# Performance work log

Measured on AMD Instinct MI355X. Metric: run time of the kernel, lower is better.

The kernel has to match this reference:

```python
import jax, jax.numpy as jnp
import numpy as np

N_HEAD = 12

def fillnan(x):
    return jnp.nan_to_num(x, nan=0.0, posinf=0.0, neginf=0.0)

def setup_inputs() -> dict:
    key = jax.random.key(0)
    k1, k2, k3 = jax.random.split(key, 3)
    B, T, C = 2, 2048, 768
    x = jax.random.normal(k1, (B, T, C), dtype=jnp.float32)
    W_attn = jax.random.normal(k2, (3 * C, C), dtype=jnp.float32) * 0.02
    W_proj = jax.random.normal(k3, (C, C), dtype=jnp.float32) * 0.02
    return {"x": x, "W_attn": W_attn, "W_proj": W_proj}

def reference(x, W_attn, W_proj):
    B, T, C = x.shape
    H = N_HEAD
    D = C // H
    # qkv projection (torch Linear: x @ W^T), then nan-sanitize
    qkv = fillnan(jnp.einsum('btc,fc->btf', x, W_attn))  # [B,T,3C]
    q, k, v = jnp.split(qkv, 3, axis=-1)
    # [B,T,C] -> [B,H,T,D]
    q = q.reshape(B, T, H, D).transpose(0, 2, 1, 3)
    k = k.reshape(B, T, H, D).transpose(0, 2, 1, 3)
    v = v.reshape(B, T, H, D).transpose(0, 2, 1, 3)
    scale = 1.0 / np.sqrt(D).astype(np.float32)
    att = jnp.einsum('bhqd,bhkd->bhqk', q, k) * scale  # [B,H,T,T]
    att = fillnan(att)
    causal = jnp.tril(jnp.ones((T, T), dtype=bool))
    att = jnp.where(causal[None, None], att, -jnp.inf)
    att = jax.nn.softmax(att, axis=-1)
    att = fillnan(att)
    y = jnp.einsum('bhqk,bhkd->bhqd', att, v)  # [B,H,T,D]
    y = fillnan(y)
    y = y.transpose(0, 2, 1, 3).reshape(B, T, C)
    y = fillnan(jnp.einsum('btc,fc->btf', y, W_proj))
    return y
```

## Files before the change

kernel.cpp:

```cpp
#include <hip/hip_runtime.h>

typedef __attribute__((ext_vector_type(8))) short bf16x8;
typedef __attribute__((ext_vector_type(4))) float f32x4;

__device__ __forceinline__ unsigned short f2b(float f) {
  union { float f; unsigned u; } v; v.f = f;
  return (unsigned short)((v.u + 0x7FFFu + ((v.u >> 16) & 1u)) >> 16);
}
__device__ __forceinline__ unsigned short f2b_fast(float f) {
  union { float f; unsigned u; } v; v.f = f;
  return (unsigned short)((v.u + 0x8000u) >> 16);
}

#define XN4   786432
#define WAN4  442368
#define WPN4  147456
__global__ void cvt_all(const float* __restrict__ x, const float* __restrict__ Wa,
                        const float* __restrict__ Wp,
                        unsigned short* __restrict__ xb, unsigned short* __restrict__ Wab,
                        unsigned short* __restrict__ Wpb) {
  int i = blockIdx.x * 256 + threadIdx.x;
  const float* src; unsigned short* dst; int off;
  if (i < XN4)            { src = x;  dst = xb;  off = i; }
  else if (i < XN4 + WAN4){ src = Wa; dst = Wab; off = i - XN4; }
  else                    { src = Wp; dst = Wpb; off = i - XN4 - WAN4; }
  float4 f = reinterpret_cast<const float4*>(src)[off];
  ushort4 o;
  o.x = f2b(f.x); o.y = f2b(f.y); o.z = f2b(f.z); o.w = f2b(f.w);
  reinterpret_cast<ushort4*>(dst)[off] = o;
}

#define BK 64

__global__ __launch_bounds__(256, 2)
void gemm_qkv(const unsigned short* __restrict__ A,
              const unsigned short* __restrict__ Bm,
              unsigned short* __restrict__ qb,
              unsigned short* __restrict__ kb_,
              unsigned short* __restrict__ vt) {
  __shared__ unsigned short As[128 * 64];
  __shared__ unsigned short Bs[128 * 64];
  const int K = 768;
  int tid = threadIdx.x;
  int wave = tid >> 6, lane = tid & 63;
  int quad = lane >> 4, l16 = lane & 15;
  int m0 = blockIdx.x * 128, n0 = blockIdx.y * 128;
  int wm = (wave & 1) * 64, wn = (wave >> 1) * 64;
  bool vswap = (n0 >= 1536);

  int srow = lane >> 3;
  int scol = ((lane & 7) ^ srow) << 3;

  f32x4 acc[4][4] = {};

  for (int k0 = 0; k0 < K; k0 += BK) {
    __syncthreads();
#pragma unroll
    for (int i = 0; i < 4; ++i) {
      int r = wave * 32 + i * 8;
      __builtin_amdgcn_global_load_lds(
          (const __attribute__((address_space(1))) unsigned int*)(A + (size_t)(m0 + r + srow) * K + k0 + scol),
          (__attribute__((address_space(3))) unsigned int*)(As + r * 64), 16, 0, 0);
      __builtin_amdgcn_global_load_lds(
          (const __attribute__((address_space(1))) unsigned int*)(Bm + (size_t)(n0 + r + srow) * K + k0 + scol),
          (__attribute__((address_space(3))) unsigned int*)(Bs + r * 64), 16, 0, 0);
    }
    __syncthreads();
#pragma unroll
    for (int kb = 0; kb < 2; ++kb) {
      int ch = (((kb << 2) | quad) ^ (l16 & 7)) << 3;
      bf16x8 af[4], bf[4];
#pragma unroll
      for (int i = 0; i < 4; ++i)
        af[i] = *reinterpret_cast<const bf16x8*>(As + (wm + i * 16 + l16) * 64 + ch);
#pragma unroll
      for (int j = 0; j < 4; ++j)
        bf[j] = *reinterpret_cast<const bf16x8*>(Bs + (wn + j * 16 + l16) * 64 + ch);
      if (!vswap) {
#pragma unroll
        for (int i = 0; i < 4; ++i)
#pragma unroll
          for (int j = 0; j < 4; ++j)
            acc[i][j] = __builtin_amdgcn_mfma_f32_16x16x32_bf16(af[i], bf[j], acc[i][j], 0, 0, 0);
      } else {
#pragma unroll
        for (int i = 0; i < 4; ++i)
#pragma unroll
          for (int j = 0; j < 4; ++j)
            acc[i][j] = __builtin_amdgcn_mfma_f32_16x16x32_bf16(bf[j], af[i], acc[i][j], 0, 0, 0);
      }
    }
  }

  const float scale2 = 0.125f * 1.44269504089f;
  if (!vswap) {
#pragma unroll
    for (int i = 0; i < 4; ++i) {
      int mbase = m0 + wm + i * 16 + quad * 4;
#pragma unroll
      for (int j = 0; j < 4; ++j) {
        int f = n0 + wn + j * 16 + l16;
        int which = f / 768;
        int f2 = f - which * 768;
        int h = f2 >> 6, d = f2 & 63;
#pragma unroll
        for (int r = 0; r < 4; ++r) {
          int m = mbase + r;
          int b = m >> 11, t = m & 2047;
          int bh = b * 12 + h;
          if (which == 0) qb[((size_t)(bh * 2048 + t)) * 64 + d] = f2b(acc[i][j][r] * scale2);
          else            kb_[((size_t)(bh * 2048 + t)) * 64 + d] = f2b(acc[i][j][r]);
        }
      }
    }
  } else {
#pragma unroll
    for (int j = 0; j < 4; ++j) {
      int fbase = n0 + wn + j * 16 + quad * 4 - 1536;
#pragma unroll
      for (int i = 0; i < 4; ++i) {
        int t_g = m0 + wm + i * 16 + l16;
        int b = t_g >> 11, t = t_g & 2047;
#pragma unroll
        for (int r = 0; r < 4; ++r) {
          int f2 = fbase + r;
          int h = f2 >> 6, d = f2 & 63;
          int bh = b * 12 + h;
          vt[((size_t)(bh * 64 + d)) * 2048 + t] = f2b(acc[i][j][r]);
        }
      }
    }
  }
}

#define CK 512

__global__ __launch_bounds__(256, 4)
void attn_part(const unsigned short* __restrict__ Qb,
               const unsigned short* __restrict__ Kb,
               const unsigned short* __restrict__ Vt,
               float* __restrict__ Oacc, float* __restrict__ Lacc) {
  __shared__ unsigned short Ks[64 * 64];
  __shared__ unsigned short Vs[64 * 64];
  __shared__ unsigned short P[4 * 32 * 64];
  const int T = 2048, D = 64;
  int wave = threadIdx.x >> 6, lane = threadIdx.x & 63;
  int quad = lane >> 4, l16 = lane & 15;

  int w = blockIdx.x;
  int bh = w / 40;
  int r = w - bh * 40;
  int b = 15;
#pragma unroll
  for (int i = 0; i < 16; ++i) {
    int nb = (i >> 2) + 1;
    if (r < nb) { b = i; break; }
    r -= nb;
  }
  int c = r;
  int q0 = b * 128;
  int qrow = q0 + wave * 32;
  int kbeg = c * CK;
  int kend = kbeg + CK; if (kend > q0 + 128) kend = q0 + 128;

  const unsigned short* Qp = Qb + (size_t)bh * T * D;
  const unsigned short* Kp = Kb + (size_t)bh * T * D;
  const unsigned short* Vp = Vt + (size_t)bh * D * T;
  unsigned short* Pw = P + wave * 32 * 64;

  int srow = lane >> 3;
  int scol = ((lane & 7) ^ srow) << 3;

  bf16x8 aq[2][2];
#pragma unroll
  for (int qi = 0; qi < 2; ++qi)
#pragma unroll
    for (int cc = 0; cc < 2; ++cc)
      aq[qi][cc] = *reinterpret_cast<const bf16x8*>(
          Qp + (qrow + qi * 16 + l16) * D + cc * 32 + quad * 8);

  bf16x8 ones;
#pragma unroll
  for (int e = 0; e < 8; ++e) ones[e] = (short)0x3F80;

  f32x4 o[2][4] = {};
  f32x4 lacc[2] = {};
  int pswr = (l16 & 7) ^ (l16 >> 3);

  for (int k0 = kbeg; k0 < kend; k0 += 64) {
    __syncthreads();
#pragma unroll
    for (int i = 0; i < 2; ++i) {
      int rr = wave * 16 + i * 8;
      __builtin_amdgcn_global_load_lds(
          (const __attribute__((address_space(1))) unsigned int*)(Kp + (size_t)(k0 + rr + srow) * D + scol),
          (__attribute__((address_space(3))) unsigned int*)(Ks + rr * 64), 16, 0, 0);
      __builtin_amdgcn_global_load_lds(
          (const __attribute__((address_space(1))) unsigned int*)(Vp + (size_t)(rr + srow) * T + k0 + scol),
          (__attribute__((address_space(3))) unsigned int*)(Vs + rr * 64), 16, 0, 0);
    }
    __syncthreads();

    if (k0 > qrow + 31) continue;

    f32x4 sacc[2][4] = {};
#pragma unroll
    for (int nt = 0; nt < 4; ++nt) {
      bf16x8 bk0 = *reinterpret_cast<const bf16x8*>(Ks + (nt * 16 + l16) * 64 + ((quad ^ (l16 & 7)) << 3));
      bf16x8 bk1 = *reinterpret_cast<const bf16x8*>(Ks + (nt * 16 + l16) * 64 + (((4 | quad) ^ (l16 & 7)) << 3));
#pragma unroll
      for (int qi = 0; qi < 2; ++qi) {
        sacc[qi][nt] = __builtin_amdgcn_mfma_f32_16x16x32_bf16(aq[qi][0], bk0, sacc[qi][nt], 0, 0, 0);
        sacc[qi][nt] = __builtin_amdgcn_mfma_f32_16x16x32_bf16(aq[qi][1], bk1, sacc[qi][nt], 0, 0, 0);
      }
    }

    if (k0 + 63 > qrow) {
#pragma unroll
      for (int qi = 0; qi < 2; ++qi)
#pragma unroll
        for (int nt = 0; nt < 4; ++nt) {
          int col = k0 + nt * 16 + l16;
#pragma unroll
          for (int rr = 0; rr < 4; ++rr) {
            int row = qrow + qi * 16 + quad * 4 + rr;
            sacc[qi][nt][rr] = (col <= row) ? sacc[qi][nt][rr] : -1e30f;
          }
        }
    }
#pragma unroll
    for (int qi = 0; qi < 2; ++qi)
#pragma unroll
      for (int nt = 0; nt < 4; ++nt)
#pragma unroll
        for (int rr = 0; rr < 4; ++rr)
          sacc[qi][nt][rr] = exp2f(sacc[qi][nt][rr]);

#pragma unroll
    for (int qi = 0; qi < 2; ++qi)
#pragma unroll
      for (int rr = 0; rr < 4; ++rr) {
        int prow = qi * 16 + quad * 4 + rr;
        int psw = (prow & 7) ^ ((prow >> 3) & 1);
#pragma unroll
        for (int nt = 0; nt < 4; ++nt)
          Pw[prow * 64 + (((nt * 2 + (l16 >> 3)) ^ psw) << 3) + (l16 & 7)] = f2b_fast(sacc[qi][nt][rr]);
      }
    __asm__ volatile("s_waitcnt lgkmcnt(0)" ::: "memory");

    bf16x8 vf[4][2];
#pragma unroll
    for (int dt = 0; dt < 4; ++dt) {
      vf[dt][0] = *reinterpret_cast<const bf16x8*>(Vs + (dt * 16 + l16) * 64 + ((quad ^ (l16 & 7)) << 3));
      vf[dt][1] = *reinterpret_cast<const bf16x8*>(Vs + (dt * 16 + l16) * 64 + (((4 | quad) ^ (l16 & 7)) << 3));
    }
#pragma unroll
    for (int qi = 0; qi < 2; ++qi) {
      bf16x8 ap0 = *reinterpret_cast<const bf16x8*>(Pw + (qi * 16 + l16) * 64 + ((quad ^ pswr) << 3));
      bf16x8 ap1 = *reinterpret_cast<const bf16x8*>(Pw + (qi * 16 + l16) * 64 + (((4 | quad) ^ pswr) << 3));
#pragma unroll
      for (int dt = 0; dt < 4; ++dt) {
        o[qi][dt] = __builtin_amdgcn_mfma_f32_16x16x32_bf16(ap0, vf[dt][0], o[qi][dt], 0, 0, 0);
        o[qi][dt] = __builtin_amdgcn_mfma_f32_16x16x32_bf16(ap1, vf[dt][1], o[qi][dt], 0, 0, 0);
      }
      lacc[qi] = __builtin_amdgcn_mfma_f32_16x16x32_bf16(ap0, ones, lacc[qi], 0, 0, 0);
      lacc[qi] = __builtin_amdgcn_mfma_f32_16x16x32_bf16(ap1, ones, lacc[qi], 0, 0, 0);
    }
  }

#pragma unroll
  for (int qi = 0; qi < 2; ++qi)
#pragma unroll
    for (int dt = 0; dt < 4; ++dt)
#pragma unroll
      for (int rr = 0; rr < 4; ++rr) {
        int row = qrow + qi * 16 + quad * 4 + rr;
        atomicAdd(&Oacc[((size_t)(bh * T + row)) * 64 + dt * 16 + l16], o[qi][dt][rr]);
      }
  if (l16 == 0) {
#pragma unroll
    for (int qi = 0; qi < 2; ++qi)
#pragma unroll
      for (int rr = 0; rr < 4; ++rr)
        atomicAdd(&Lacc[bh * T + qrow + qi * 16 + quad * 4 + rr], lacc[qi][rr]);
  }
}

__global__ __launch_bounds__(256, 2)
void gemm_proj(const float* __restrict__ Oacc, const float* __restrict__ Lacc,
               const unsigned short* __restrict__ Wpb, float* __restrict__ out) {
  __shared__ unsigned short As[64 * 64];
  __shared__ unsigned short Bs[128 * 64];
  int tid = threadIdx.x;
  int wave = tid >> 6, lane = tid & 63;
  int quad = lane >> 4, l16 = lane & 15;
  int m0 = blockIdx.x * 64, n0 = blockIdx.y * 128;
  int wm = (wave & 1) * 32, wn = (wave >> 1) * 64;

  int srow = lane >> 3;
  int scol = ((lane & 7) ^ srow) << 3;

  int arow = tid >> 2;
  int acg = (tid & 3) * 2;
  int t_g = m0 + arow;
  int bb = t_g >> 11, tt = t_g & 2047;
  int asw = arow & 7;

  f32x4 acc[2][4] = {};

  for (int k0 = 0; k0 < 768; k0 += BK) {
    int h = k0 >> 6;
    const float* arp = Oacc + ((size_t)((bb * 12 + h) * 2048 + tt)) * 64 + acg * 8;
    float rl = 1.0f / Lacc[(bb * 12 + h) * 2048 + tt];
    float4 a0 = reinterpret_cast<const float4*>(arp)[0];
    float4 a1 = reinterpret_cast<const float4*>(arp)[1];
    float4 a2 = reinterpret_cast<const float4*>(arp)[2];
    float4 a3 = reinterpret_cast<const float4*>(arp)[3];

    __syncthreads();
#pragma unroll
    for (int i = 0; i < 4; ++i) {
      int r = wave * 32 + i * 8;
      __builtin_amdgcn_global_load_lds(
          (const __attribute__((address_space(1))) unsigned int*)(Wpb + (size_t)(n0 + r + srow) * 768 + k0 + scol),
          (__attribute__((address_space(3))) unsigned int*)(Bs + r * 64), 16, 0, 0);
    }
    bf16x8 p0, p1;
    p0[0] = (short)f2b(a0.x * rl); p0[1] = (short)f2b(a0.y * rl);
    p0[2] = (short)f2b(a0.z * rl); p0[3] = (short)f2b(a0.w * rl);
    p0[4] = (short)f2b(a1.x * rl); p0[5] = (short)f2b(a1.y * rl);
    p0[6] = (short)f2b(a1.z * rl); p0[7] = (short)f2b(a1.w * rl);
    p1[0] = (short)f2b(a2.x * rl); p1[1] = (short)f2b(a2.y * rl);
    p1[2] = (short)f2b(a2.z * rl); p1[3] = (short)f2b(a2.w * rl);
    p1[4] = (short)f2b(a3.x * rl); p1[5] = (short)f2b(a3.y * rl);
    p1[6] = (short)f2b(a3.z * rl); p1[7] = (short)f2b(a3.w * rl);
    *reinterpret_cast<bf16x8*>(As + arow * 64 + ((acg ^ asw) << 3)) = p0;
    *reinterpret_cast<bf16x8*>(As + arow * 64 + (((acg + 1) ^ asw) << 3)) = p1;
    __syncthreads();

#pragma unroll
    for (int kb = 0; kb < 2; ++kb) {
      int ch = (((kb << 2) | quad) ^ (l16 & 7)) << 3;
      bf16x8 af[2], bf[4];
#pragma unroll
      for (int i = 0; i < 2; ++i)
        af[i] = *reinterpret_cast<const bf16x8*>(As + (wm + i * 16 + l16) * 64 + ch);
#pragma unroll
      for (int j = 0; j < 4; ++j)
        bf[j] = *reinterpret_cast<const bf16x8*>(Bs + (wn + j * 16 + l16) * 64 + ch);
#pragma unroll
      for (int i = 0; i < 2; ++i)
#pragma unroll
        for (int j = 0; j < 4; ++j)
          acc[i][j] = __builtin_amdgcn_mfma_f32_16x16x32_bf16(af[i], bf[j], acc[i][j], 0, 0, 0);
    }
  }

#pragma unroll
  for (int i = 0; i < 2; ++i) {
    int mbase = m0 + wm + i * 16 + quad * 4;
#pragma unroll
    for (int j = 0; j < 4; ++j) {
      int col = n0 + wn + j * 16 + l16;
#pragma unroll
      for (int r = 0; r < 4; ++r)
        out[(size_t)(mbase + r) * 768 + col] = acc[i][j][r];
    }
  }
}

extern "C" void kernel_launch(void* const* d_in, const int* in_sizes, int n_in,
                              void* d_out, int out_size, void* d_ws, size_t ws_size,
                              hipStream_t stream) {
  const float* x  = (const float*)d_in[0];
  const float* Wa = (const float*)d_in[1];
  const float* Wp = (const float*)d_in[2];
  float* out = (float*)d_out;

  unsigned short* ws = (unsigned short*)d_ws;
  unsigned short* xb  = ws;
  unsigned short* Wab = xb  + 3145728;
  unsigned short* Wpb = Wab + 1769472;
  unsigned short* Qb  = Wpb + 589824;
  unsigned short* Kb  = Qb  + 3145728;
  unsigned short* Vt  = Kb  + 3145728;
  float*          Oacc = (float*)(Vt + 3145728);
  float*          Lacc = Oacc + 3145728;

  hipMemsetAsync(Oacc, 0, (3145728 + 49152) * sizeof(float), stream);

  cvt_all<<<(XN4 + WAN4 + WPN4) / 256, 256, 0, stream>>>(x, Wa, Wp, xb, Wab, Wpb);

  gemm_qkv<<<dim3(32, 18), 256, 0, stream>>>(xb, Wab, Qb, Kb, Vt);

  attn_part<<<960, 256, 0, stream>>>(Qb, Kb, Vt, Oacc, Lacc);

  gemm_proj<<<dim3(64, 6), 256, 0, stream>>>(Oacc, Lacc, Wpb, out);
}
```

Before: 185.2 us.

## Double-buffer LDS in all GEMM and attention kernels; finer attention split with XCD mapping

Adds double-buffered shared-memory staging to the QKV GEMM, attention and projection GEMM kernels. Each kernel now prefetches the next K tile while computing on the current one, which removes one barrier per iteration. The attention key-chunk size is halved (CK 256), giving 1728 blocks, and blockIdx is remapped so heads are grouped per XCD for L2 locality. The risks are higher LDS use, which lowers occupancy (launch bounds reduced to 3), and more partial-sum atomics into Oacc from the finer split.

```diff
diff --git a/kernel.cpp b/kernel.cpp
--- a/kernel.cpp
+++ b/kernel.cpp
@@ -30,16 +30,14 @@
   reinterpret_cast<ushort4*>(dst)[off] = o;
 }
 
-#define BK 64
-
 __global__ __launch_bounds__(256, 2)
 void gemm_qkv(const unsigned short* __restrict__ A,
               const unsigned short* __restrict__ Bm,
               unsigned short* __restrict__ qb,
               unsigned short* __restrict__ kb_,
               unsigned short* __restrict__ vt) {
-  __shared__ unsigned short As[128 * 64];
-  __shared__ unsigned short Bs[128 * 64];
+  __shared__ unsigned short As[2][128 * 64];
+  __shared__ unsigned short Bs[2][128 * 64];
   const int K = 768;
   int tid = threadIdx.x;
   int wave = tid >> 6, lane = tid & 63;
@@ -51,31 +49,36 @@
   int srow = lane >> 3;
   int scol = ((lane & 7) ^ srow) << 3;
 
-  f32x4 acc[4][4] = {};
-
-  for (int k0 = 0; k0 < K; k0 += BK) {
-    __syncthreads();
+  auto stage = [&](int k0, int buf) {
 #pragma unroll
     for (int i = 0; i < 4; ++i) {
       int r = wave * 32 + i * 8;
       __builtin_amdgcn_global_load_lds(
           (const __attribute__((address_space(1))) unsigned int*)(A + (size_t)(m0 + r + srow) * K + k0 + scol),
-          (__attribute__((address_space(3))) unsigned int*)(As + r * 64), 16, 0, 0);
+          (__attribute__((address_space(3))) unsigned int*)(&As[buf][r * 64]), 16, 0, 0);
       __builtin_amdgcn_global_load_lds(
           (const __attribute__((address_space(1))) unsigned int*)(Bm + (size_t)(n0 + r + srow) * K + k0 + scol),
-          (__attribute__((address_space(3))) unsigned int*)(Bs + r * 64), 16, 0, 0);
-    }
+          (__attribute__((address_space(3))) unsigned int*)(&Bs[buf][r * 64]), 16, 0, 0);
+    }
+  };
+
+  f32x4 acc[4][4] = {};
+  stage(0, 0);
+  int cur = 0;
+
+  for (int k0 = 0; k0 < K; k0 += 64) {
     __syncthreads();
+    if (k0 + 64 < K) stage(k0 + 64, cur ^ 1);
 #pragma unroll
     for (int kb = 0; kb < 2; ++kb) {
       int ch = (((kb << 2) | quad) ^ (l16 & 7)) << 3;
       bf16x8 af[4], bf[4];
 #pragma unroll
       for (int i = 0; i < 4; ++i)
-        af[i] = *reinterpret_cast<const bf16x8*>(As + (wm + i * 16 + l16) * 64 + ch);
+        af[i] = *reinterpret_cast<const bf16x8*>(&As[cur][(wm + i * 16 + l16) * 64 + ch]);
 #pragma unroll
       for (int j = 0; j < 4; ++j)
-        bf[j] = *reinterpret_cast<const bf16x8*>(Bs + (wn + j * 16 + l16) * 64 + ch);
+        bf[j] = *reinterpret_cast<const bf16x8*>(&Bs[cur][(wn + j * 16 + l16) * 64 + ch]);
       if (!vswap) {
 #pragma unroll
         for (int i = 0; i < 4; ++i)
@@ -90,6 +93,7 @@
             acc[i][j] = __builtin_amdgcn_mfma_f32_16x16x32_bf16(bf[j], af[i], acc[i][j], 0, 0, 0);
       }
     }
+    cur ^= 1;
   }
 
   const float scale2 = 0.125f * 1.44269504089f;
@@ -133,27 +137,29 @@
   }
 }
 
-#define CK 512
-
-__global__ __launch_bounds__(256, 4)
+#define CK 256
+
+__global__ __launch_bounds__(256, 3)
 void attn_part(const unsigned short* __restrict__ Qb,
                const unsigned short* __restrict__ Kb,
                const unsigned short* __restrict__ Vt,
                float* __restrict__ Oacc, float* __restrict__ Lacc) {
-  __shared__ unsigned short Ks[64 * 64];
-  __shared__ unsigned short Vs[64 * 64];
+  __shared__ unsigned short Ks[2][64 * 64];
+  __shared__ unsigned short Vs[2][64 * 64];
   __shared__ unsigned short P[4 * 32 * 64];
   const int T = 2048, D = 64;
   int wave = threadIdx.x >> 6, lane = threadIdx.x & 63;
   int quad = lane >> 4, l16 = lane & 15;
 
-  int w = blockIdx.x;
-  int bh = w / 40;
-  int r = w - bh * 40;
+  int flat = blockIdx.x;
+  int xcd = flat & 7;
+  int ix = flat >> 3;
+  int bh = xcd * 3 + ix / 72;
+  int r = ix % 72;
   int b = 15;
 #pragma unroll
   for (int i = 0; i < 16; ++i) {
-    int nb = (i >> 2) + 1;
+    int nb = (i >> 1) + 1;
     if (r < nb) { b = i; break; }
     r -= nb;
   }
@@ -171,101 +177,109 @@
   int srow = lane >> 3;
   int scol = ((lane & 7) ^ srow) << 3;
 
-  bf16x8 aq[2][2];
-#pragma unroll
-  for (int qi = 0; qi < 2; ++qi)
-#pragma unroll
-    for (int cc = 0; cc < 2; ++cc)
-      aq[qi][cc] = *reinterpret_cast<const bf16x8*>(
-          Qp + (qrow + qi * 16 + l16) * D + cc * 32 + quad * 8);
-
-  bf16x8 ones;
-#pragma unroll
-  for (int e = 0; e < 8; ++e) ones[e] = (short)0x3F80;
-
-  f32x4 o[2][4] = {};
-  f32x4 lacc[2] = {};
-  int pswr = (l16 & 7) ^ (l16 >> 3);
-
-  for (int k0 = kbeg; k0 < kend; k0 += 64) {
-    __syncthreads();
+  auto stage = [&](int k0, int buf) {
 #pragma unroll
     for (int i = 0; i < 2; ++i) {
       int rr = wave * 16 + i * 8;
       __builtin_amdgcn_global_load_lds(
           (const __attribute__((address_space(1))) unsigned int*)(Kp + (size_t)(k0 + rr + srow) * D + scol),
-          (__attribute__((address_space(3))) unsigned int*)(Ks + rr * 64), 16, 0, 0);
+          (__attribute__((address_space(3))) unsigned int*)(&Ks[buf][rr * 64]), 16, 0, 0);
       __builtin_amdgcn_global_load_lds(
           (const __attribute__((address_space(1))) unsigned int*)(Vp + (size_t)(rr + srow) * T + k0 + scol),
-          (__attribute__((address_space(3))) unsigned int*)(Vs + rr * 64), 16, 0, 0);
-    }
+          (__attribute__((address_space(3))) unsigned int*)(&Vs[buf][rr * 64]), 16, 0, 0);
+    }
+  };
+
+  bf16x8 aq[2][2];
+#pragma unroll
+  for (int qi = 0; qi < 2; ++qi)
+#pragma unroll
+    for (int cc = 0; cc < 2; ++cc)
+      aq[qi][cc] = *reinterpret_cast<const bf16x8*>(
+          Qp + (qrow + qi * 16 + l16) * D + cc * 32 + quad * 8);
+
+  bf16x8 ones;
+#pragma unroll
+  for (int e = 0; e < 8; ++e) ones[e] = (short)0x3F80;
+
+  f32x4 o[2][4] = {};
+  f32x4 lacc[2] = {};
+  int pswr = (l16 & 7) ^ (l16 >> 3);
+
+  stage(kbeg, 0);
+  int cur = 0;
+
+  for (int k0 = kbeg; k0 < kend; k0 += 64) {
     __syncthreads();
-
-    if (k0 > qrow + 31) continue;
-
-    f32x4 sacc[2][4] = {};
-#pragma unroll
-    for (int nt = 0; nt < 4; ++nt) {
-      bf16x8 bk0 = *reinterpret_cast<const bf16x8*>(Ks + (nt * 16 + l16) * 64 + ((quad ^ (l16 & 7)) << 3));
-      bf16x8 bk1 = *reinterpret_cast<const bf16x8*>(Ks + (nt * 16 + l16) * 64 + (((4 | quad) ^ (l16 & 7)) << 3));
+    if (k0 + 64 < kend) stage(k0 + 64, cur ^ 1);
+
+    if (k0 <= qrow + 31) {
+      f32x4 sacc[2][4] = {};
+#pragma unroll
+      for (int nt = 0; nt < 4; ++nt) {
+        bf16x8 bk0 = *reinterpret_cast<const bf16x8*>(&Ks[cur][(nt * 16 + l16) * 64 + ((quad ^ (l16 & 7)) << 3)]);
+        bf16x8 bk1 = *reinterpret_cast<const bf16x8*>(&Ks[cur][(nt * 16 + l16) * 64 + (((4 | quad) ^ (l16 & 7)) << 3)]);
+#pragma unroll
+        for (int qi = 0; qi < 2; ++qi) {
+          sacc[qi][nt] = __builtin_amdgcn_mfma_f32_16x16x32_bf16(aq[qi][0], bk0, sacc[qi][nt], 0, 0, 0);
+          sacc[qi][nt] = __builtin_amdgcn_mfma_f32_16x16x32_bf16(aq[qi][1], bk1, sacc[qi][nt], 0, 0, 0);
+        }
+      }
+
+      if (k0 + 63 > qrow) {
+#pragma unroll
+        for (int qi = 0; qi < 2; ++qi)
+#pragma unroll
+          for (int nt = 0; nt < 4; ++nt) {
+            int col = k0 + nt * 16 + l16;
+#pragma unroll
+            for (int rr = 0; rr < 4; ++rr) {
+              int row = qrow + qi * 16 + quad * 4 + rr;
+              sacc[qi][nt][rr] = (col <= row) ? sacc[qi][nt][rr] : -1e30f;
+            }
+          }
+      }
+#pragma unroll
+      for (int qi = 0; qi < 2; ++qi)
+#pragma unroll
+        for (int nt = 0; nt < 4; ++nt)
+#pragma unroll
+          for (int rr = 0; rr < 4; ++rr)
+            sacc[qi][nt][rr] = exp2f(sacc[qi][nt][rr]);
+
+#pragma unroll
+      for (int qi = 0; qi < 2; ++qi)
+#pragma unroll
+        for (int rr = 0; rr < 4; ++rr) {
+          int prow = qi * 16 + quad * 4 + rr;
+          int psw = (prow & 7) ^ ((prow >> 3) & 1);
+#pragma unroll
+          for (int nt = 0; nt < 4; ++nt)
+            Pw[prow * 64 + (((nt * 2 + (l16 >> 3)) ^ psw) << 3) + (l16 & 7)] = f2b_fast(sacc[qi][nt][rr]);
+        }
+      __asm__ volatile("s_waitcnt lgkmcnt(0)" ::: "memory");
+
+      bf16x8 vf[4][2];
+#pragma unroll
+      for (int dt = 0; dt < 4; ++dt) {
+        vf[dt][0] = *reinterpret_cast<const bf16x8*>(&Vs[cur][(dt * 16 + l16) * 64 + ((quad ^ (l16 & 7)) << 3)]);
+        vf[dt][1] = *reinterpret_cast<const bf16x8*>(&Vs[cur][(dt * 16 + l16) * 64 + (((4 | quad) ^ (l16 & 7)) << 3)]);
+      }
 #pragma unroll
       for (int qi = 0; qi < 2; ++qi) {
-        sacc[qi][nt] = __builtin_amdgcn_mfma_f32_16x16x32_bf16(aq[qi][0], bk0, sacc[qi][nt], 0, 0, 0);
-        sacc[qi][nt] = __builtin_amdgcn_mfma_f32_16x16x32_bf16(aq[qi][1], bk1, sacc[qi][nt], 0, 0, 0);
-      }
-    }
-
-    if (k0 + 63 > qrow) {
-#pragma unroll
-      for (int qi = 0; qi < 2; ++qi)
-#pragma unroll
-        for (int nt = 0; nt < 4; ++nt) {
-          int col = k0 + nt * 16 + l16;
-#pragma unroll
-          for (int rr = 0; rr < 4; ++rr) {
-            int row = qrow + qi * 16 + quad * 4 + rr;
-            sacc[qi][nt][rr] = (col <= row) ? sacc[qi][nt][rr] : -1e30f;
-          }
+        bf16x8 ap0 = *reinterpret_cast<const bf16x8*>(Pw + (qi * 16 + l16) * 64 + ((quad ^ pswr) << 3));
+        bf16x8 ap1 = *reinterpret_cast<const bf16x8*>(Pw + (qi * 16 + l16) * 64 + (((4 | quad) ^ pswr) << 3));
+#pragma unroll
+        for (int dt = 0; dt < 4; ++dt) {
+          o[qi][dt] = __builtin_amdgcn_mfma_f32_16x16x32_bf16(ap0, vf[dt][0], o[qi][dt], 0, 0, 0);
+          o[qi][dt] = __builtin_amdgcn_mfma_f32_16x16x32_bf16(ap1, vf[dt][1], o[qi][dt], 0, 0, 0);
         }
-    }
-#pragma unroll
-    for (int qi = 0; qi < 2; ++qi)
-#pragma unroll
-      for (int nt = 0; nt < 4; ++nt)
-#pragma unroll
-        for (int rr = 0; rr < 4; ++rr)
-          sacc[qi][nt][rr] = exp2f(sacc[qi][nt][rr]);
-
-#pragma unroll
-    for (int qi = 0; qi < 2; ++qi)
-#pragma unroll
-      for (int rr = 0; rr < 4; ++rr) {
-        int prow = qi * 16 + quad * 4 + rr;
-        int psw = (prow & 7) ^ ((prow >> 3) & 1);
-#pragma unroll
-        for (int nt = 0; nt < 4; ++nt)
-          Pw[prow * 64 + (((nt * 2 + (l16 >> 3)) ^ psw) << 3) + (l16 & 7)] = f2b_fast(sacc[qi][nt][rr]);
-      }
-    __asm__ volatile("s_waitcnt lgkmcnt(0)" ::: "memory");
-
-    bf16x8 vf[4][2];
-#pragma unroll
-    for (int dt = 0; dt < 4; ++dt) {
-      vf[dt][0] = *reinterpret_cast<const bf16x8*>(Vs + (dt * 16 + l16) * 64 + ((quad ^ (l16 & 7)) << 3));
-      vf[dt][1] = *reinterpret_cast<const bf16x8*>(Vs + (dt * 16 + l16) * 64 + (((4 | quad) ^ (l16 & 7)) << 3));
-    }
-#pragma unroll
-    for (int qi = 0; qi < 2; ++qi) {
-      bf16x8 ap0 = *reinterpret_cast<const bf16x8*>(Pw + (qi * 16 + l16) * 64 + ((quad ^ pswr) << 3));
-      bf16x8 ap1 = *reinterpret_cast<const bf16x8*>(Pw + (qi * 16 + l16) * 64 + (((4 | quad) ^ pswr) << 3));
-#pragma unroll
-      for (int dt = 0; dt < 4; ++dt) {
-        o[qi][dt] = __builtin_amdgcn_mfma_f32_16x16x32_bf16(ap0, vf[dt][0], o[qi][dt], 0, 0, 0);
-        o[qi][dt] = __builtin_amdgcn_mfma_f32_16x16x32_bf16(ap1, vf[dt][1], o[qi][dt], 0, 0, 0);
-      }
-      lacc[qi] = __builtin_amdgcn_mfma_f32_16x16x32_bf16(ap0, ones, lacc[qi], 0, 0, 0);
-      lacc[qi] = __builtin_amdgcn_mfma_f32_16x16x32_bf16(ap1, ones, lacc[qi], 0, 0, 0);
-    }
+        lacc[qi] = __builtin_amdgcn_mfma_f32_16x16x32_bf16(ap0, ones, lacc[qi], 0, 0, 0);
+        lacc[qi] = __builtin_amdgcn_mfma_f32_16x16x32_bf16(ap1, ones, lacc[qi], 0, 0, 0);
+      }
+      __asm__ volatile("" ::: "memory");
+    }
+    cur ^= 1;
   }
 
 #pragma unroll
@@ -289,8 +303,8 @@
 __global__ __launch_bounds__(256, 2)
 void gemm_proj(const float* __restrict__ Oacc, const float* __restrict__ Lacc,
                const unsigned short* __restrict__ Wpb, float* __restrict__ out) {
-  __shared__ unsigned short As[64 * 64];
-  __shared__ unsigned short Bs[128 * 64];
+  __shared__ unsigned short As[2][64 * 64];
+  __shared__ unsigned short Bs[2][128 * 64];
   int tid = threadIdx.x;
   int wave = tid >> 6, lane = tid & 63;
   int quad = lane >> 4, l16 = lane & 15;
@@ -306,54 +320,72 @@
   int bb = t_g >> 11, tt = t_g & 2047;
   int asw = arow & 7;
 
-  f32x4 acc[2][4] = {};
-
-  for (int k0 = 0; k0 < 768; k0 += BK) {
-    int h = k0 >> 6;
-    const float* arp = Oacc + ((size_t)((bb * 12 + h) * 2048 + tt)) * 64 + acg * 8;
-    float rl = 1.0f / Lacc[(bb * 12 + h) * 2048 + tt];
-    float4 a0 = reinterpret_cast<const float4*>(arp)[0];
-    float4 a1 = reinterpret_cast<const float4*>(arp)[1];
-    float4 a2 = reinterpret_cast<const float4*>(arp)[2];
-    float4 a3 = reinterpret_cast<const float4*>(arp)[3];
-
-    __syncthreads();
+  auto stageB = [&](int k0, int buf) {
 #pragma unroll
     for (int i = 0; i < 4; ++i) {
       int r = wave * 32 + i * 8;
       __builtin_amdgcn_global_load_lds(
           (const __attribute__((address_space(1))) unsigned int*)(Wpb + (size_t)(n0 + r + srow) * 768 + k0 + scol),
-          (__attribute__((address_space(3))) unsigned int*)(Bs + r * 64), 16, 0, 0);
-    }
+          (__attribute__((address_space(3))) unsigned int*)(&Bs[buf][r * 64]), 16, 0, 0);
+    }
+  };
+  auto loadA = [&](int k0, float4* a, float& rl) {
+    int h = k0 >> 6;
+    const float* arp = Oacc + ((size_t)((bb * 12 + h) * 2048 + tt)) * 64 + acg * 8;
+    rl = 1.0f / Lacc[(bb * 12 + h) * 2048 + tt];
+    a[0] = reinterpret_cast<const float4*>(arp)[0];
+    a[1] = reinterpret_cast<const float4*>(arp)[1];
+    a[2] = reinterpret_cast<const float4*>(arp)[2];
+    a[3] = reinterpret_cast<const float4*>(arp)[3];
+  };
+  auto writeA = [&](const float4* a, float rl, int buf) {
     bf16x8 p0, p1;
-    p0[0] = (short)f2b(a0.x * rl); p0[1] = (short)f2b(a0.y * rl);
-    p0[2] = (short)f2b(a0.z * rl); p0[3] = (short)f2b(a0.w * rl);
-    p0[4] = (short)f2b(a1.x * rl); p0[5] = (short)f2b(a1.y * rl);
-    p0[6] = (short)f2b(a1.z * rl); p0[7] = (short)f2b(a1.w * rl);
-    p1[0] = (short)f2b(a2.x * rl); p1[1] = (short)f2b(a2.y * rl);
-    p1[2] = (short)f2b(a2.z * rl); p1[3] = (short)f2b(a2.w * rl);
-    p1[4] = (short)f2b(a3.x * rl); p1[5] = (short)f2b(a3.y * rl);
-    p1[6] = (short)f2b(a3.z * rl); p1[7] = (short)f2b(a3.w * rl);
-    *reinterpret_cast<bf16x8*>(As + arow * 64 + ((acg ^ asw) << 3)) = p0;
-    *reinterpret_cast<bf16x8*>(As + arow * 64 + (((acg + 1) ^ asw) << 3)) = p1;
+    p0[0] = (short)f2b(a[0].x * rl); p0[1] = (short)f2b(a[0].y * rl);
+    p0[2] = (short)f2b(a[0].z * rl); p0[3] = (short)f2b(a[0].w * rl);
+    p0[4] = (short)f2b(a[1].x * rl); p0[5] = (short)f2b(a[1].y * rl);
+    p0[6] = (short)f2b(a[1].z * rl); p0[7] = (short)f2b(a[1].w * rl);
+    p1[0] = (short)f2b(a[2].x * rl); p1[1] = (short)f2b(a[2].y * rl);
+    p1[2] = (short)f2b(a[2].z * rl); p1[3] = (short)f2b(a[2].w * rl);
+    p1[4] = (short)f2b(a[3].x * rl); p1[5] = (short)f2b(a[3].y * rl);
+    p1[6] = (short)f2b(a[3].z * rl); p1[7] = (short)f2b(a[3].w * rl);
+    *reinterpret_cast<bf16x8*>(&As[buf][arow * 64 + ((acg ^ asw) << 3)]) = p0;
+    *reinterpret_cast<bf16x8*>(&As[buf][arow * 64 + (((acg + 1) ^ asw) << 3)]) = p1;
+  };
+
+  f32x4 acc[2][4] = {};
+
+  float4 aP[4], aN[4];
+  float rlP, rlN;
+  stageB(0, 0);
+  loadA(0, aP, rlP);
+  loadA(64, aN, rlN);
+  writeA(aP, rlP, 0);
+  int cur = 0;
+
+  for (int k0 = 0; k0 < 768; k0 += 64) {
     __syncthreads();
-
+    if (k0 + 64 < 768) {
+      stageB(k0 + 64, cur ^ 1);
+      writeA(aN, rlN, cur ^ 1);
+      if (k0 + 128 < 768) loadA(k0 + 128, aN, rlN);
+    }
 #pragma unroll
     for (int kb = 0; kb < 2; ++kb) {
       int ch = (((kb << 2) | quad) ^ (l16 & 7)) << 3;
       bf16x8 af[2], bf[4];
 #pragma unroll
       for (int i = 0; i < 2; ++i)
-        af[i] = *reinterpret_cast<const bf16x8*>(As + (wm + i * 16 + l16) * 64 + ch);
+        af[i] = *reinterpret_cast<const bf16x8*>(&As[cur][(wm + i * 16 + l16) * 64 + ch]);
 #pragma unroll
       for (int j = 0; j < 4; ++j)
-        bf[j] = *reinterpret_cast<const bf16x8*>(Bs + (wn + j * 16 + l16) * 64 + ch);
+        bf[j] = *reinterpret_cast<const bf16x8*>(&Bs[cur][(wn + j * 16 + l16) * 64 + ch]);
 #pragma unroll
       for (int i = 0; i < 2; ++i)
 #pragma unroll
         for (int j = 0; j < 4; ++j)
           acc[i][j] = __builtin_amdgcn_mfma_f32_16x16x32_bf16(af[i], bf[j], acc[i][j], 0, 0, 0);
     }
+    cur ^= 1;
   }
 
 #pragma unroll
@@ -393,7 +425,7 @@
 
   gemm_qkv<<<dim3(32, 18), 256, 0, stream>>>(xb, Wab, Qb, Kb, Vt);
 
-  attn_part<<<960, 256, 0, stream>>>(Qb, Kb, Vt, Oacc, Lacc);
+  attn_part<<<1728, 256, 0, stream>>>(Qb, Kb, Vt, Oacc, Lacc);
 
   gemm_proj<<<dim3(64, 6), 256, 0, stream>>>(Oacc, Lacc, Wpb, out);
 }
```

New measurement: 180.8 us. -2.4%, faster.
